# Performance work log

Hardware: AMD Instinct MI355X
Metric: run time of the kernel (lower is better)

## Reference

```python
import jax, jax.numpy as jnp
import numpy as np

B, S, H, NH = 8, 1024, 768, 12
I = 3072
HD = H // NH  # 64


def setup_inputs() -> dict:
    key = jax.random.key(0)
    ks = jax.random.split(key, 6)
    w = lambda k, shape: jax.random.normal(k, shape, jnp.float32) * 0.02
    return {
        "x": jax.random.normal(ks[0], (B, S, H), jnp.float32),
        "ln1_g": jnp.ones((H,), jnp.float32),
        "ln1_b": jnp.zeros((H,), jnp.float32),
        "qkv_w": w(ks[1], (H, 3 * H)),
        "qkv_b": jnp.zeros((3 * H,), jnp.float32),
        "proj_w": w(ks[2], (H, H)),
        "proj_b": jnp.zeros((H,), jnp.float32),
        "ln2_g": jnp.ones((H,), jnp.float32),
        "ln2_b": jnp.zeros((H,), jnp.float32),
        "fc1_w": w(ks[3], (H, I)),
        "fc1_b": jnp.zeros((I,), jnp.float32),
        "fc2_w": w(ks[4], (I, H)),
        "fc2_b": jnp.zeros((H,), jnp.float32),
    }


def _layernorm(x, g, b, eps=1e-5):
    m = x.mean(-1, keepdims=True)
    v = x.var(-1, keepdims=True)  # biased variance, matches torch LayerNorm
    return (x - m) * jax.lax.rsqrt(v + eps) * g + b


def _new_gelu(x):
    c = np.float32(np.sqrt(2.0 / np.pi))
    return 0.5 * x * (1.0 + jnp.tanh(c * (x + 0.044715 * x * x * x)))


def reference(x, ln1_g, ln1_b, qkv_w, qkv_b, proj_w, proj_b,
              ln2_g, ln2_b, fc1_w, fc1_b, fc2_w, fc2_b):
    # --- attention sublayer (pre-LN) ---
    h = _layernorm(x, ln1_g, ln1_b)                     # [B,S,H]
    qkv = h @ qkv_w + qkv_b                             # [B,S,3H]
    q, k, v = jnp.split(qkv, 3, axis=-1)
    q = q.reshape(B, S, NH, HD).transpose(0, 2, 1, 3)   # [B,NH,S,HD]
    k = k.reshape(B, S, NH, HD).transpose(0, 2, 1, 3)
    v = v.reshape(B, S, NH, HD).transpose(0, 2, 1, 3)
    scores = jnp.einsum('bhtd,bhsd->bhts', q, k) / np.float32(np.sqrt(HD))
    probs = jax.nn.softmax(scores, axis=-1)             # [B,NH,S,S]
    attn = jnp.einsum('bhts,bhsd->bhtd', probs, v)      # [B,NH,S,HD]
    attn = attn.transpose(0, 2, 1, 3).reshape(B, S, H)
    attn = attn @ proj_w + proj_b
    x = x + attn
    # --- MLP sublayer (pre-LN) ---
    h2 = _layernorm(x, ln2_g, ln2_b)
    m = _new_gelu(h2 @ fc1_w + fc1_b) @ fc2_w + fc2_b
    return x + m
```

## Files before the change

### kernel.cpp

```cpp
#include <hip/hip_runtime.h>
#include <hip/hip_bf16.h>


typedef __attribute__((ext_vector_type(8))) short bf16x8;
typedef __attribute__((ext_vector_type(4))) float f32x4;
typedef const __attribute__((address_space(3))) char* lds_cp;

#define MFMA16(a, b, c) __builtin_amdgcn_mfma_f32_16x16x32_bf16((a), (b), (c), 0, 0, 0)

#define DSR(dst, addr, off) \
    asm volatile("ds_read_b128 %0, %1 offset:" #off : "=v"(dst) : "v"(addr))
#define WAITV4 asm volatile("s_waitcnt vmcnt(4)" ::: "memory")
#define WAITV0 asm volatile("s_waitcnt vmcnt(0)" ::: "memory")
#define WAITLG asm volatile("s_waitcnt lgkmcnt(0)" ::: "memory")
#define SCHEDB __builtin_amdgcn_sched_barrier(0)

__device__ inline short f2bf(float x) {
    __hip_bfloat16 h = __float2bfloat16(x);
    return *reinterpret_cast<short*>(&h);
}

__device__ inline void gload_lds16(const void* g, void* lds) {
    __builtin_amdgcn_global_load_lds(
        (const __attribute__((address_space(1))) unsigned int*)g,
        (__attribute__((address_space(3))) unsigned int*)lds,
        16, 0, 0);
}

__global__ __launch_bounds__(256) void transpose_w(
    const float* __restrict__ W, short* __restrict__ Wt, int K, int N) {
    __shared__ float tile[32][33];
    const int tx = threadIdx.x & 31, ty = threadIdx.x >> 5;
    const int n0 = blockIdx.x * 32, k0 = blockIdx.y * 32;
#pragma unroll
    for (int i = 0; i < 4; ++i)
        tile[ty + i * 8][tx] = W[(size_t)(k0 + ty + i * 8) * N + n0 + tx];
    __syncthreads();
#pragma unroll
    for (int i = 0; i < 4; ++i)
        Wt[(size_t)(n0 + ty + i * 8) * K + k0 + tx] = f2bf(tile[tx][ty + i * 8]);
}

__global__ __launch_bounds__(256) void ln_k(
    const float* __restrict__ x, const float* __restrict__ g,
    const float* __restrict__ b, short* __restrict__ out) {
    const int row = blockIdx.x;
    const int tid = threadIdx.x;
    const float* xr = x + (size_t)row * 768;
    float v[3];
    float s = 0.f, sq = 0.f;
#pragma unroll
    for (int i = 0; i < 3; ++i) {
        v[i] = xr[tid + i * 256];
        s += v[i];
        sq += v[i] * v[i];
    }
#pragma unroll
    for (int off = 32; off >= 1; off >>= 1) {
        s += __shfl_xor(s, off);
        sq += __shfl_xor(sq, off);
    }
    __shared__ float ss[4], ssq[4];
    const int wid = tid >> 6;
    if ((tid & 63) == 0) { ss[wid] = s; ssq[wid] = sq; }
    __syncthreads();
    s = ss[0] + ss[1] + ss[2] + ss[3];
    sq = ssq[0] + ssq[1] + ssq[2] + ssq[3];
    const float mean = s * (1.0f / 768.0f);
    const float var = sq * (1.0f / 768.0f) - mean * mean;
    const float rstd = rsqrtf(var + 1e-5f);
    short* outr = out + (size_t)row * 768;
#pragma unroll
    for (int i = 0; i < 3; ++i) {
        const int c = tid + i * 256;
        outr[c] = f2bf((v[i] - mean) * rstd * g[c] + b[c]);
    }
}

enum { MODE_BF16 = 0, MODE_QKV = 1, MODE_F32RES = 2, MODE_GELU = 3 };

template <int MODE>
__global__ __launch_bounds__(256) void gemm3p(
    const short* __restrict__ A, const short* __restrict__ Wt,
    const float* __restrict__ bias, const float* __restrict__ resid,
    float* __restrict__ outf, short* __restrict__ outh,
    short* __restrict__ Qo, short* __restrict__ Ko, short* __restrict__ Vto,
    int M, int N, int K) {
    __shared__ __attribute__((aligned(128))) short Al[3][4096];
    __shared__ __attribute__((aligned(128))) short Bl[3][4096];
    const int tid = threadIdx.x;
    const int lane = tid & 63;
    const int w = tid >> 6;
    const int wm = w >> 1, wn = w & 1;
    const int m0 = blockIdx.x * 128, n0 = blockIdx.y * 128;

    f32x4 acc[4][4] = {};

    const int srow = tid >> 2;
    const int scol = ((tid & 3) * 8) ^ (((tid >> 2) & 3) << 3);
    const short* Abase = A + (size_t)(m0 + srow) * K + scol;
    const short* Bbase = Wt + (size_t)(n0 + srow) * K + scol;
    const size_t K64 = (size_t)K * 64;
    short* const AlF = &Al[0][0];
    short* const BlF = &Bl[0][0];

    auto stageT = [&](int boS, int k0s) {
        gload_lds16(Abase + k0s,       AlF + boS + w * 512);
        gload_lds16(Abase + K64 + k0s, AlF + boS + 2048 + w * 512);
        gload_lds16(Bbase + k0s,       BlF + boS + w * 512);
        gload_lds16(Bbase + K64 + k0s, BlF + boS + 2048 + w * 512);
    };

    const int lrow = lane & 15;
    const int lcolswz = ((lane >> 4) * 16) ^ ((lane & 3) << 4);
    const int aoff = wm * 4096 + lrow * 64 + lcolswz;
    const int boff = wn * 4096 + lrow * 64 + lcolswz;
    const lds_cp AlB = (lds_cp)AlF;
    const lds_cp BlB = (lds_cp)BlF;

    const int NT = K >> 5;

    stageT(0, 0);
    stageT(4096, 32);
    WAITV4;
    SCHEDB;
    __builtin_amdgcn_s_barrier();

    int bo = 0, bo1 = 8192, bo2 = 16384;
    for (int t = 0; t < NT; ++t) {
        const lds_cp Ab = AlB + (bo + aoff);
        const lds_cp Bb = BlB + (bo + boff);
        bf16x8 av0, av1, av2, av3, bv0, bv1, bv2, bv3;
        DSR(av0, Ab, 0);
        DSR(av1, Ab, 1024);
        DSR(av2, Ab, 2048);
        DSR(av3, Ab, 3072);
        DSR(bv0, Bb, 0);
        DSR(bv1, Bb, 1024);
        DSR(bv2, Bb, 2048);
        DSR(bv3, Bb, 3072);

        int ts = t + 2;
        if (ts > NT - 1) ts = NT - 1;
        stageT(bo2 >> 1, ts << 5);
        WAITV4;
        SCHEDB;
        __builtin_amdgcn_s_barrier();
        WAITLG;
        SCHEDB;

        __builtin_amdgcn_s_setprio(1);
        {
            bf16x8 av[4] = {av0, av1, av2, av3};
            bf16x8 bv[4] = {bv0, bv1, bv2, bv3};
#pragma unroll
            for (int mi = 0; mi < 4; ++mi)
#pragma unroll
                for (int ni = 0; ni < 4; ++ni)
                    acc[mi][ni] = MFMA16(av[mi], bv[ni], acc[mi][ni]);
        }
        __builtin_amdgcn_s_setprio(0);
        __builtin_amdgcn_s_barrier();

        const int tmp = bo; bo = bo1; bo1 = bo2; bo2 = tmp;
    }
    WAITV0;

#pragma unroll
    for (int mi = 0; mi < 4; ++mi) {
#pragma unroll
        for (int ni = 0; ni < 4; ++ni) {
#pragma unroll
            for (int r = 0; r < 4; ++r) {
                const int row = m0 + wm * 64 + mi * 16 + (lane >> 4) * 4 + r;
                const int col = n0 + wn * 64 + ni * 16 + (lane & 15);
                float v = acc[mi][ni][r] + bias[col];
                if constexpr (MODE == MODE_BF16) {
                    outh[(size_t)row * N + col] = f2bf(v);
                } else if constexpr (MODE == MODE_GELU) {
                    const float u = 0.7978845608028654f * (v + 0.044715f * v * v * v);
                    const float gl = v / (1.0f + __expf(-2.0f * u));
                    outh[(size_t)row * N + col] = f2bf(gl);
                } else if constexpr (MODE == MODE_F32RES) {
                    outf[(size_t)row * N + col] = v + resid[(size_t)row * N + col];
                } else {
                    const int bb = row >> 10, s = row & 1023;
                    if (col < 768) {
                        const int hh = col >> 6, d = col & 63;
                        Qo[(((size_t)(bb * 12 + hh)) * 1024 + s) * 64 + d] = f2bf(v * 0.125f);
                    } else if (col < 1536) {
                        const int c2 = col - 768;
                        const int hh = c2 >> 6, d = c2 & 63;
                        Ko[(((size_t)(bb * 12 + hh)) * 1024 + s) * 64 + d] = f2bf(v);
                    } else {
                        const int c2 = col - 1536;
                        const int hh = c2 >> 6, d = c2 & 63;
                        Vto[(((size_t)(bb * 12 + hh)) * 64 + d) * 1024 + s] = f2bf(v);
                    }
                }
            }
        }
    }
}

__global__ __launch_bounds__(256) void attn_k(
    const short* __restrict__ Q, const short* __restrict__ Kg,
    const short* __restrict__ Vtg, short* __restrict__ out) {
    __shared__ __attribute__((aligned(128))) short Kl[2][64 * 64];
    __shared__ __attribute__((aligned(128))) short Vl[2][64 * 64];
    __shared__ __attribute__((aligned(128))) short Pl[4][16 * 64];
    const int tid = threadIdx.x, lane = tid & 63, w = tid >> 6;
    const int swz = (blockIdx.x & 7) * 192 + (blockIdx.x >> 3);
    const int qt = swz & 15, bh = swz >> 4;
    const int b = bh / 12, h = bh % 12;
    const int q0 = qt * 64 + w * 16;
    const int l15 = lane & 15, g = lane >> 4;

    bf16x8 aq[2];
    const short* Qb = Q + ((size_t)bh * 1024 + q0) * 64;
#pragma unroll
    for (int kk = 0; kk < 2; ++kk)
        aq[kk] = *(const bf16x8*)&Qb[(size_t)l15 * 64 + kk * 32 + g * 8];

    float m_run[4], l_run[4];
    f32x4 o[4] = {};
#pragma unroll
    for (int r = 0; r < 4; ++r) { m_run[r] = -1e30f; l_run[r] = 0.f; }

    const short* Kb = Kg + (size_t)bh * 1024 * 64;
    const short* Vb = Vtg + (size_t)bh * 64 * 1024;

    const int srr = tid >> 3;
    const int spp = (tid & 7) * 8;
    const int ssc = spp ^ ((srr & 7) << 3);
    auto stage = [&](int buf, int kv0) {
        gload_lds16(Kb + (size_t)(kv0 + srr) * 64 + ssc,      &Kl[buf][w * 512]);
        gload_lds16(Kb + (size_t)(kv0 + 32 + srr) * 64 + ssc, &Kl[buf][2048 + w * 512]);
        gload_lds16(Vb + (size_t)srr * 1024 + kv0 + ssc,      &Vl[buf][w * 512]);
        gload_lds16(Vb + (size_t)(srr + 32) * 1024 + kv0 + ssc, &Vl[buf][2048 + w * 512]);
    };

    stage(0, 0);
    __syncthreads();

    int buf = 0;
    for (int t = 0; t < 16; ++t) {
        const lds_cp KB = (lds_cp)&Kl[buf][0];
        const lds_cp VB = (lds_cp)&Vl[buf][0];

        bf16x8 kb[4][2];
#pragma unroll
        for (int nk = 0; nk < 4; ++nk) {
            const int R = nk * 16 + l15;
            const int c0 = (g * 8) ^ ((R & 7) << 3);
            const lds_cp a0 = KB + R * 128 + c0 * 2;
            const lds_cp a1 = KB + R * 128 + (c0 ^ 32) * 2;
            DSR(kb[nk][0], a0, 0);
            DSR(kb[nk][1], a1, 0);
        }

        if (t < 15) stage(buf ^ 1, (t + 1) * 64);

        WAITLG;
        SCHEDB;

        f32x4 sc4[4];
#pragma unroll
        for (int nk = 0; nk < 4; ++nk) {
            f32x4 z = {};
            z = MFMA16(aq[0], kb[nk][0], z);
            z = MFMA16(aq[1], kb[nk][1], z);
            sc4[nk] = z;
        }

        float alpha[4], padd[4][4];
#pragma unroll
        for (int r = 0; r < 4; ++r) {
            float ml = fmaxf(fmaxf(sc4[0][r], sc4[1][r]), fmaxf(sc4[2][r], sc4[3][r]));
#pragma unroll
            for (int mk = 1; mk <= 8; mk <<= 1) ml = fmaxf(ml, __shfl_xor(ml, mk));
            const float mn = fmaxf(m_run[r], ml);
            alpha[r] = __expf(m_run[r] - mn);
            m_run[r] = mn;
            float rsum = 0.f;
#pragma unroll
            for (int nk = 0; nk < 4; ++nk) {
                padd[nk][r] = __expf(sc4[nk][r] - mn);
                rsum += padd[nk][r];
            }
#pragma unroll
            for (int mk = 1; mk <= 8; mk <<= 1) rsum += __shfl_xor(rsum, mk);
            l_run[r] = l_run[r] * alpha[r] + rsum;
#pragma unroll
            for (int dn = 0; dn < 4; ++dn) o[dn][r] *= alpha[r];
        }

#pragma unroll
        for (int nk = 0; nk < 4; ++nk)
#pragma unroll
            for (int r = 0; r < 4; ++r) {
                const int rr = g * 4 + r, cc = nk * 16 + l15;
                Pl[w][rr * 64 + (cc ^ ((rr & 7) << 3))] = f2bf(padd[nk][r]);
            }
        bf16x8 pa[2];
#pragma unroll
        for (int kk = 0; kk < 2; ++kk)
            pa[kk] = *(const bf16x8*)&Pl[w][l15 * 64 + ((kk * 32 + g * 8) ^ ((l15 & 7) << 3))];

        bf16x8 vb[4][2];
#pragma unroll
        for (int dn = 0; dn < 4; ++dn) {
            const int R = dn * 16 + l15;
            const int c0 = (g * 8) ^ ((R & 7) << 3);
            const lds_cp a0 = VB + R * 128 + c0 * 2;
            const lds_cp a1 = VB + R * 128 + (c0 ^ 32) * 2;
            DSR(vb[dn][0], a0, 0);
            DSR(vb[dn][1], a1, 0);
        }
        WAITLG;
        SCHEDB;

#pragma unroll
        for (int dn = 0; dn < 4; ++dn) {
            o[dn] = MFMA16(pa[0], vb[dn][0], o[dn]);
            o[dn] = MFMA16(pa[1], vb[dn][1], o[dn]);
        }

        __syncthreads();
        buf ^= 1;
    }

#pragma unroll
    for (int r = 0; r < 4; ++r) {
        const float rl = __builtin_amdgcn_rcpf(l_run[r]);
        const int srow = q0 + g * 4 + r;
#pragma unroll
        for (int dn = 0; dn < 4; ++dn)
            out[((size_t)(b * 1024) + srow) * 768 + h * 64 + dn * 16 + l15] =
                f2bf(o[dn][r] * rl);
    }
}

extern "C" void kernel_launch(void* const* d_in, const int* in_sizes, int n_in,
                              void* d_out, int out_size, void* d_ws, size_t ws_size,
                              hipStream_t stream) {
    const float* x      = (const float*)d_in[0];
    const float* ln1_g  = (const float*)d_in[1];
    const float* ln1_b  = (const float*)d_in[2];
    const float* qkv_w  = (const float*)d_in[3];
    const float* qkv_b  = (const float*)d_in[4];
    const float* proj_w = (const float*)d_in[5];
    const float* proj_b = (const float*)d_in[6];
    const float* ln2_g  = (const float*)d_in[7];
    const float* ln2_b  = (const float*)d_in[8];
    const float* fc1_w  = (const float*)d_in[9];
    const float* fc1_b  = (const float*)d_in[10];
    const float* fc2_w  = (const float*)d_in[11];
    const float* fc2_b  = (const float*)d_in[12];
    float* outp = (float*)d_out;

    char* ws = (char*)d_ws;
    size_t off = 0;
    auto alloc = [&](size_t bytes) {
        char* p = ws + off;
        off = (off + bytes + 255) & ~(size_t)255;
        return p;
    };
    short* wt_qkv  = (short*)alloc(2304ull * 768 * 2);
    short* wt_proj = (short*)alloc(768ull * 768 * 2);
    short* wt_fc1  = (short*)alloc(3072ull * 768 * 2);
    short* wt_fc2  = (short*)alloc(768ull * 3072 * 2);
    short* hbuf    = (short*)alloc(8192ull * 768 * 2);
    short* Qb      = (short*)alloc(8192ull * 768 * 2);
    short* Kbuf    = (short*)alloc(8192ull * 768 * 2);
    short* Vtb     = (short*)alloc(8192ull * 768 * 2);
    short* attnb   = (short*)alloc(8192ull * 768 * 2);
    float* x2      = (float*)alloc(8192ull * 768 * 4);
    short* mfc     = Qb;
    (void)ws_size; (void)in_sizes; (void)n_in; (void)out_size;

    transpose_w<<<dim3(2304 / 32, 768 / 32), 256, 0, stream>>>(qkv_w, wt_qkv, 768, 2304);
    transpose_w<<<dim3(768 / 32, 768 / 32), 256, 0, stream>>>(proj_w, wt_proj, 768, 768);
    transpose_w<<<dim3(3072 / 32, 768 / 32), 256, 0, stream>>>(fc1_w, wt_fc1, 768, 3072);
    transpose_w<<<dim3(768 / 32, 3072 / 32), 256, 0, stream>>>(fc2_w, wt_fc2, 3072, 768);

    ln_k<<<8192, 256, 0, stream>>>(x, ln1_g, ln1_b, hbuf);
    gemm3p<MODE_QKV><<<dim3(64, 18), 256, 0, stream>>>(
        hbuf, wt_qkv, qkv_b, nullptr, nullptr, nullptr, Qb, Kbuf, Vtb, 8192, 2304, 768);
    attn_k<<<1536, 256, 0, stream>>>(Qb, Kbuf, Vtb, attnb);
    gemm3p<MODE_F32RES><<<dim3(64, 6), 256, 0, stream>>>(
        attnb, wt_proj, proj_b, x, x2, nullptr, nullptr, nullptr, nullptr, 8192, 768, 768);

    ln_k<<<8192, 256, 0, stream>>>(x2, ln2_g, ln2_b, hbuf);
    gemm3p<MODE_GELU><<<dim3(64, 24), 256, 0, stream>>>(
        hbuf, wt_fc1, fc1_b, nullptr, nullptr, mfc, nullptr, nullptr, nullptr, 8192, 3072, 768);
    gemm3p<MODE_F32RES><<<dim3(64, 6), 256, 0, stream>>>(
        mfc, wt_fc2, fc2_b, x2, outp, nullptr, nullptr, nullptr, nullptr, 8192, 768, 3072);
}
```

Before: 308.6 us.

## Swap MFMA operands in attention so each lane owns one query row

The QK^T and PV MFMAs now take their operands in swapped order, so the accumulator is transposed and each lane holds a single query row across four key columns. Per-row softmax statistics become scalars, and the max and sum reductions need only two cross-lane shuffles instead of four per row. P is packed to bf16 with v_cvt_pk_bf16_f32 and written to LDS as 8-byte vector stores, and the output is written the same way. This cuts shuffle, conversion and scattered-store work in the softmax inner loop, with some risk of new LDS bank conflicts from the changed P store pattern.

```diff
diff --git a/kernel.cpp b/kernel.cpp
--- a/kernel.cpp
+++ b/kernel.cpp
@@ -14,6 +14,8 @@
 #define WAITV0 asm volatile("s_waitcnt vmcnt(0)" ::: "memory")
 #define WAITLG asm volatile("s_waitcnt lgkmcnt(0)" ::: "memory")
 #define SCHEDB __builtin_amdgcn_sched_barrier(0)
+#define CVTPK(d, lo, hi) \
+    asm("v_cvt_pk_bf16_f32 %0, %1, %2" : "=v"(d) : "v"(lo), "v"(hi))
 
 __device__ inline short f2bf(float x) {
     __hip_bfloat16 h = __float2bfloat16(x);
@@ -222,10 +224,8 @@
     for (int kk = 0; kk < 2; ++kk)
         aq[kk] = *(const bf16x8*)&Qb[(size_t)l15 * 64 + kk * 32 + g * 8];
 
-    float m_run[4], l_run[4];
+    float m_run = -1e30f, l_run = 0.f;
     f32x4 o[4] = {};
-#pragma unroll
-    for (int r = 0; r < 4; ++r) { m_run[r] = -1e30f; l_run[r] = 0.f; }
 
     const short* Kb = Kg + (size_t)bh * 1024 * 64;
     const short* Vb = Vtg + (size_t)bh * 64 * 1024;
@@ -234,9 +234,9 @@
     const int spp = (tid & 7) * 8;
     const int ssc = spp ^ ((srr & 7) << 3);
     auto stage = [&](int buf, int kv0) {
-        gload_lds16(Kb + (size_t)(kv0 + srr) * 64 + ssc,      &Kl[buf][w * 512]);
-        gload_lds16(Kb + (size_t)(kv0 + 32 + srr) * 64 + ssc, &Kl[buf][2048 + w * 512]);
-        gload_lds16(Vb + (size_t)srr * 1024 + kv0 + ssc,      &Vl[buf][w * 512]);
+        gload_lds16(Kb + (size_t)(kv0 + srr) * 64 + ssc,        &Kl[buf][w * 512]);
+        gload_lds16(Kb + (size_t)(kv0 + 32 + srr) * 64 + ssc,   &Kl[buf][2048 + w * 512]);
+        gload_lds16(Vb + (size_t)srr * 1024 + kv0 + ssc,        &Vl[buf][w * 512]);
         gload_lds16(Vb + (size_t)(srr + 32) * 1024 + kv0 + ssc, &Vl[buf][2048 + w * 512]);
     };
 
@@ -268,40 +268,45 @@
 #pragma unroll
         for (int nk = 0; nk < 4; ++nk) {
             f32x4 z = {};
-            z = MFMA16(aq[0], kb[nk][0], z);
-            z = MFMA16(aq[1], kb[nk][1], z);
+            z = MFMA16(kb[nk][0], aq[0], z);
+            z = MFMA16(kb[nk][1], aq[1], z);
             sc4[nk] = z;
         }
 
-        float alpha[4], padd[4][4];
-#pragma unroll
-        for (int r = 0; r < 4; ++r) {
-            float ml = fmaxf(fmaxf(sc4[0][r], sc4[1][r]), fmaxf(sc4[2][r], sc4[3][r]));
-#pragma unroll
-            for (int mk = 1; mk <= 8; mk <<= 1) ml = fmaxf(ml, __shfl_xor(ml, mk));
-            const float mn = fmaxf(m_run[r], ml);
-            alpha[r] = __expf(m_run[r] - mn);
-            m_run[r] = mn;
-            float rsum = 0.f;
-#pragma unroll
-            for (int nk = 0; nk < 4; ++nk) {
+        float ml = sc4[0][0];
+#pragma unroll
+        for (int nk = 0; nk < 4; ++nk)
+#pragma unroll
+            for (int r = 0; r < 4; ++r) ml = fmaxf(ml, sc4[nk][r]);
+        ml = fmaxf(ml, __shfl_xor(ml, 16));
+        ml = fmaxf(ml, __shfl_xor(ml, 32));
+        const float mn = fmaxf(m_run, ml);
+        const float alpha = __expf(m_run - mn);
+        m_run = mn;
+        float padd[4][4];
+        float rsum = 0.f;
+#pragma unroll
+        for (int nk = 0; nk < 4; ++nk)
+#pragma unroll
+            for (int r = 0; r < 4; ++r) {
                 padd[nk][r] = __expf(sc4[nk][r] - mn);
                 rsum += padd[nk][r];
             }
-#pragma unroll
-            for (int mk = 1; mk <= 8; mk <<= 1) rsum += __shfl_xor(rsum, mk);
-            l_run[r] = l_run[r] * alpha[r] + rsum;
-#pragma unroll
-            for (int dn = 0; dn < 4; ++dn) o[dn][r] *= alpha[r];
-        }
-
-#pragma unroll
-        for (int nk = 0; nk < 4; ++nk)
-#pragma unroll
-            for (int r = 0; r < 4; ++r) {
-                const int rr = g * 4 + r, cc = nk * 16 + l15;
-                Pl[w][rr * 64 + (cc ^ ((rr & 7) << 3))] = f2bf(padd[nk][r]);
-            }
+        rsum += __shfl_xor(rsum, 16);
+        rsum += __shfl_xor(rsum, 32);
+        l_run = l_run * alpha + rsum;
+#pragma unroll
+        for (int dn = 0; dn < 4; ++dn) o[dn] *= alpha;
+
+#pragma unroll
+        for (int nk = 0; nk < 4; ++nk) {
+            unsigned u0, u1;
+            CVTPK(u0, padd[nk][0], padd[nk][1]);
+            CVTPK(u1, padd[nk][2], padd[nk][3]);
+            const int cc = (nk * 16 + g * 4) ^ ((l15 & 7) << 3);
+            uint2 uv; uv.x = u0; uv.y = u1;
+            *reinterpret_cast<uint2*>(&Pl[w][l15 * 64 + cc]) = uv;
+        }
         bf16x8 pa[2];
 #pragma unroll
         for (int kk = 0; kk < 2; ++kk)
@@ -322,22 +327,25 @@
 
 #pragma unroll
         for (int dn = 0; dn < 4; ++dn) {
-            o[dn] = MFMA16(pa[0], vb[dn][0], o[dn]);
-            o[dn] = MFMA16(pa[1], vb[dn][1], o[dn]);
+            o[dn] = MFMA16(vb[dn][0], pa[0], o[dn]);
+            o[dn] = MFMA16(vb[dn][1], pa[1], o[dn]);
         }
 
         __syncthreads();
         buf ^= 1;
     }
 
-#pragma unroll
-    for (int r = 0; r < 4; ++r) {
-        const float rl = __builtin_amdgcn_rcpf(l_run[r]);
-        const int srow = q0 + g * 4 + r;
-#pragma unroll
-        for (int dn = 0; dn < 4; ++dn)
-            out[((size_t)(b * 1024) + srow) * 768 + h * 64 + dn * 16 + l15] =
-                f2bf(o[dn][r] * rl);
+    const float rl = __builtin_amdgcn_rcpf(l_run);
+    short* orow = out + ((size_t)(b * 1024) + q0 + l15) * 768 + h * 64;
+#pragma unroll
+    for (int dn = 0; dn < 4; ++dn) {
+        unsigned u0, u1;
+        const float v0 = o[dn][0] * rl, v1 = o[dn][1] * rl;
+        const float v2 = o[dn][2] * rl, v3 = o[dn][3] * rl;
+        CVTPK(u0, v0, v1);
+        CVTPK(u1, v2, v3);
+        uint2 uv; uv.x = u0; uv.y = u1;
+        *reinterpret_cast<uint2*>(&orow[dn * 16 + g * 4]) = uv;
     }
 }
 
```

New measurement: 280.3 us. 9.2% less time.
